# Kernel optimization log

Hardware: AMD Instinct MI355X
Metric: run time of the kernel (lower is better)

Reference implementation:

```python
import jax, jax.numpy as jnp
import numpy as np
import math

D_MODEL = 1024
NUM_HEADS = 16
D_K = D_MODEL // NUM_HEADS
B, NQ, NK = 2, 2048, 2048


def setup_inputs() -> dict:
    key = jax.random.key(0)
    ks = jax.random.split(key, 14)
    s = 1.0 / math.sqrt(D_MODEL)
    inp = {
        "query": jax.random.normal(ks[0], (B, NQ, D_MODEL), jnp.float32),
        "key": jax.random.normal(ks[1], (B, NK, D_MODEL), jnp.float32),
        "value": jax.random.normal(ks[2], (B, NK, D_MODEL), jnp.float32),
        "mask": jax.random.randint(ks[3], (B, NK), 0, 2, jnp.int32),
        "attn_bias": jax.random.normal(ks[4], (B, NQ, NK), jnp.float32),
        "w_q": jax.random.normal(ks[5], (D_MODEL, D_MODEL), jnp.float32) * s,
        "b_q": jnp.zeros((D_MODEL,), jnp.float32),
        "w_k": jax.random.normal(ks[6], (D_MODEL, D_MODEL), jnp.float32) * s,
        "b_k": jnp.zeros((D_MODEL,), jnp.float32),
        "w_v": jax.random.normal(ks[7], (D_MODEL, D_MODEL), jnp.float32) * s,
        "b_v": jnp.zeros((D_MODEL,), jnp.float32),
        "w_o": jax.random.normal(ks[8], (D_MODEL, D_MODEL), jnp.float32) * s,
        "b_o": jnp.zeros((D_MODEL,), jnp.float32),
    }
    return inp


def reference(query, key, value, mask, attn_bias, w_q, b_q, w_k, b_k, w_v, b_v, w_o, b_o):
    # Linear projections (torch Linear: x @ W^T + b), reshape to [B, H, N, d_k]
    def proj(x, w, b, n):
        return (x @ w.T + b).reshape(x.shape[0], n, NUM_HEADS, D_K).transpose(0, 2, 1, 3)

    Q = proj(query, w_q, b_q, query.shape[1])   # [B,H,Nq,dk]
    K = proj(key, w_k, b_k, key.shape[1])       # [B,H,Nk,dk]
    V = proj(value, w_v, b_v, value.shape[1])   # [B,H,Nk,dk]

    scores = jnp.einsum("bhqd,bhkd->bhqk", Q, K) / math.sqrt(D_K)
    scores = scores + attn_bias[:, None, :, :]           # bias broadcast over heads
    pad = (mask[:, None, None, :] == 0)                   # [B,1,1,Nk]
    scores = jnp.where(pad, jnp.float32(-1e9), scores)
    attn = jax.nn.softmax(scores, axis=-1)                # dropout is identity (eval)
    out = jnp.einsum("bhqk,bhkd->bhqd", attn, V)          # [B,H,Nq,dk]
    out = out.transpose(0, 2, 1, 3).reshape(query.shape[0], query.shape[1], D_MODEL)
    return out @ w_o.T + b_o
```

## Files before the change

kernel.cpp:

```cpp
#include <hip/hip_runtime.h>


typedef short bf16x8 __attribute__((ext_vector_type(8)));
typedef short bf16x4 __attribute__((ext_vector_type(4)));
typedef float f32x4 __attribute__((ext_vector_type(4)));
typedef float f32x16 __attribute__((ext_vector_type(16)));
typedef int i32x4 __attribute__((ext_vector_type(4)));
typedef unsigned short u16;
typedef unsigned short u16x8 __attribute__((ext_vector_type(8)));
typedef unsigned short u16x4 __attribute__((ext_vector_type(4)));

#define MFMA16(a, b, c) __builtin_amdgcn_mfma_f32_16x16x32_bf16((a), (b), (c), 0, 0, 0)
#define MFMA32(a, b, c) __builtin_amdgcn_mfma_f32_32x32x16_bf16((a), (b), (c), 0, 0, 0)
#define GLD16(gp, lp)                                                     \
  __builtin_amdgcn_global_load_lds(                                       \
      (const __attribute__((address_space(1))) void*)(gp),                \
      (__attribute__((address_space(3))) void*)(lp), 16, 0, 0)

#define WAITVM_BAR(N) asm volatile("s_waitcnt vmcnt(" #N ")\ns_barrier" ::: "memory")
#define BAR() asm volatile("s_barrier" ::: "memory")

#if __has_builtin(__builtin_amdgcn_exp2f)
#define EXP2(x) __builtin_amdgcn_exp2f(x)
#else
#define EXP2(x) exp2f(x)
#endif

__device__ __forceinline__ u16 f2bf(float f) {
  union { float f; unsigned u; } v; v.f = f;
  return (u16)((v.u + 0x7fffu + ((v.u >> 16) & 1u)) >> 16);
}
__device__ __forceinline__ unsigned pk2(float x, float y) {
  union { float f; unsigned u; } a, b;
  a.f = x; b.f = y;
  return ((a.u + 0x8000u) >> 16) | ((b.u + 0x8000u) & 0xffff0000u);
}
__device__ __forceinline__ void pl32swap(unsigned& a, unsigned& b) {
  asm("v_permlane32_swap_b32 %0, %1" : "+v"(a), "+v"(b));
}

struct ConvDesc { const float* src; u16* dst; int n; };
struct ConvArgs { ConvDesc d[7]; };

__device__ __forceinline__ void biasprep_body(const float* __restrict__ bias,
                                              const int* __restrict__ mask,
                                              u16* __restrict__ out, int i) {
  const int o0 = i * 16;
  const int rowg = o0 >> 11;
  const int b = rowg >> 11;
  const int off = o0 & 2047;
  const int c = off >> 5;
  const int hi = (off >> 4) & 1;
  const float* src = bias + (size_t)rowg * 2048 + c * 32 + hi * 4;
  const int* msk = mask + b * 2048 + c * 32 + hi * 4;
  u16x8 w0 = {}, w1 = {};
#pragma unroll
  for (int t = 0; t < 4; t++) {
    f32x4 v = *(const f32x4*)(src + t * 8);
    i32x4 m = *(const i32x4*)(msk + t * 8);
#pragma unroll
    for (int j = 0; j < 4; j++) {
      u16 val = (m[j] != 0) ? f2bf(v[j] * 1.44269504f) : (u16)0xFF80;
      if (t < 2) w0[t * 4 + j] = val;
      else       w1[(t - 2) * 4 + j] = val;
    }
  }
  *(u16x8*)(out + o0) = w0;
  *(u16x8*)(out + o0 + 8) = w1;
}

__global__ __launch_bounds__(256)
void k_prep(ConvArgs a, const float* __restrict__ bias,
            const int* __restrict__ mask, u16* __restrict__ bout) {
  if (blockIdx.y == 7) {
    biasprep_body(bias, mask, bout, blockIdx.x * 256 + threadIdx.x);
    return;
  }
  ConvDesc cd = a.d[blockIdx.y];
  int i = (blockIdx.x * 256 + threadIdx.x) * 8;
  if (i >= cd.n) return;
  const float4* s = (const float4*)(cd.src + i);
  float4 f0 = s[0], f1 = s[1];
  u16x8 o;
  o[0] = f2bf(f0.x); o[1] = f2bf(f0.y); o[2] = f2bf(f0.z); o[3] = f2bf(f0.w);
  o[4] = f2bf(f1.x); o[5] = f2bf(f1.y); o[6] = f2bf(f1.z); o[7] = f2bf(f1.w);
  *(u16x8*)(cd.dst + i) = o;
}

__global__ __launch_bounds__(256)
void k_biasprep(const float* __restrict__ bias, const int* __restrict__ mask,
                u16* __restrict__ out) {
  biasprep_body(bias, mask, out, blockIdx.x * 256 + threadIdx.x);
}

template <int MF>
__device__ __forceinline__ void gemm_impl(const u16* __restrict__ A,
                                          const u16* __restrict__ Bw,
                                          const float* __restrict__ bias,
                                          void* __restrict__ outp, int mode,
                                          float oscale) {
  __shared__ u16 As[2][MF * 1024];
  __shared__ u16 Bs[2][4096];
  const int tid = threadIdx.x;
  const int lane = tid & 63;
  const int wv = tid >> 6;
  const int wr = wv >> 1, wc = wv & 1;
  const int m0 = blockIdx.y * (MF * 32), n0 = blockIdx.x * 128;

  f32x4 acc[MF][4] = {};

  const int s0 = tid, s1 = 256 + tid;
  const int r0 = s0 >> 2, c0 = (s0 & 3) ^ (r0 & 3);
  const int r1 = s1 >> 2, c1 = (s1 & 3) ^ (r1 & 3);
  const u16* gA0 = A + (size_t)(m0 + r0) * 1024 + c0 * 8;
  const u16* gA1 = A + (size_t)(m0 + r1) * 1024 + c1 * 8;
  const u16* gB0 = Bw + (size_t)(n0 + r0) * 1024 + c0 * 8;
  const u16* gB1 = Bw + (size_t)(n0 + r1) * 1024 + c1 * 8;
  u16* lA0 = &As[0][(tid & ~63) * 8];
  u16* lB0 = &Bs[0][(tid & ~63) * 8];

  GLD16(gA0, lA0);
  if constexpr (MF == 4) GLD16(gA1, lA0 + 2048);
  GLD16(gB0, lB0);
  GLD16(gB1, lB0 + 2048);
  WAITVM_BAR(0);

#define GSTEP(BUF, K0)                                                     \
  {                                                                        \
    const int nk = ((K0) + 32) & 1023;                                     \
    GLD16(gA0 + nk, lA0 + ((BUF) ^ 1) * (MF * 1024));                      \
    if constexpr (MF == 4)                                                 \
      GLD16(gA1 + nk, lA0 + 2048 + ((BUF) ^ 1) * (MF * 1024));             \
    GLD16(gB0 + nk, lB0 + ((BUF) ^ 1) * 4096);                             \
    GLD16(gB1 + nk, lB0 + 2048 + ((BUF) ^ 1) * 4096);                      \
    if constexpr (MF == 4) { WAITVM_BAR(4); } else { WAITVM_BAR(3); }      \
    bf16x8 af[MF], bfr[4];                                                 \
    _Pragma("unroll")                                                      \
    for (int mi = 0; mi < MF; mi++) {                                      \
      int row = wr * (MF * 16) + mi * 16 + (lane & 15);                    \
      int byt = row * 64 + (((lane >> 4) * 16) ^ ((row & 3) << 4));        \
      af[mi] = *(const bf16x8*)((const char*)&As[BUF][0] + byt);           \
    }                                                                      \
    _Pragma("unroll")                                                      \
    for (int ni = 0; ni < 4; ni++) {                                       \
      int row = wc * 64 + ni * 16 + (lane & 15);                           \
      int byt = row * 64 + (((lane >> 4) * 16) ^ ((row & 3) << 4));        \
      bfr[ni] = *(const bf16x8*)((const char*)&Bs[BUF][0] + byt);          \
    }                                                                      \
    __builtin_amdgcn_s_setprio(1);                                         \
    _Pragma("unroll")                                                      \
    for (int mi = 0; mi < MF; mi++)                                        \
      _Pragma("unroll")                                                    \
      for (int ni = 0; ni < 4; ni++)                                       \
        acc[mi][ni] = MFMA16(af[mi], bfr[ni], acc[mi][ni]);                \
    __builtin_amdgcn_s_setprio(0);                                         \
    BAR();                                                                 \
  }

  for (int k0 = 0; k0 < 1024; k0 += 64) {
    GSTEP(0, k0)
    GSTEP(1, k0 + 32)
  }
#undef GSTEP

#pragma unroll
  for (int ni = 0; ni < 4; ni++) {
    int n = n0 + wc * 64 + ni * 16 + (lane & 15);
    float bv = bias[n];
#pragma unroll
    for (int mi = 0; mi < MF; mi++) {
      int mb = m0 + wr * (MF * 16) + mi * 16 + (lane >> 4) * 4;
      if (mode == 2) {
        float* O = (float*)outp;
#pragma unroll
        for (int r = 0; r < 4; r++)
          O[(size_t)(mb + r) * 1024 + n] = (acc[mi][ni][r] + bv) * oscale;
      } else if (mode == 0) {
        u16* O = (u16*)outp;
        int b = mb >> 11, q = mb & 2047;
        int h = n >> 6, dk = n & 63;
        size_t base = ((size_t)(b * 16 + h) * 2048 + q) * 64 + dk;
#pragma unroll
        for (int r = 0; r < 4; r++)
          O[base + (size_t)r * 64] = f2bf((acc[mi][ni][r] + bv) * oscale);
      } else {
        u16* O = (u16*)outp;
        int b = mb >> 11, kv = mb & 2047;
        int h = n >> 6, dk = n & 63;
        u16x4 pk;
#pragma unroll
        for (int r = 0; r < 4; r++) pk[r] = f2bf((acc[mi][ni][r] + bv) * oscale);
        *(u16x4*)((u16*)O + ((size_t)((b * 16 + h) * 64 + dk)) * 2048 + kv) = pk;
      }
    }
  }
}

struct GemmDesc { const u16* A; const u16* W; const float* bias; void* out;
                  int mode; float oscale; };
struct Gemm3 { GemmDesc d[3]; };

__global__ __launch_bounds__(256, 3) void k_gemm_qkv(Gemm3 g3) {
  GemmDesc gd = g3.d[blockIdx.z];
  gemm_impl<4>(gd.A, gd.W, gd.bias, gd.out, gd.mode, gd.oscale);
}
__global__ __launch_bounds__(256, 2)
void k_gemm_o(const u16* __restrict__ A, const u16* __restrict__ W,
              const float* __restrict__ bias, float* __restrict__ out) {
  gemm_impl<2>(A, W, bias, out, 2, 1.0f);
}

__global__ __launch_bounds__(256, 2)
void k_attn(const u16* __restrict__ Qb, const u16* __restrict__ Kb,
            const u16* __restrict__ Vt, const u16* __restrict__ BiasE,
            u16* __restrict__ Ob) {
  __shared__ u16 Ks[2][128 * 64];
  __shared__ u16 Vs[2][64 * 128];

  const int tid = threadIdx.x, lane = tid & 63, w = tid >> 6;
  const int l31 = lane & 31, hi2 = lane >> 5;
  const int bid = blockIdx.x;
  const int xcd = bid & 7, rr = bid >> 3;
  const int qt = rr & 15;
  const int pr = xcd + 8 * (rr >> 4);
  const int b = pr >> 4, h = pr & 15;
  const int q0 = qt * 128;
  const size_t bh = (size_t)(b * 16 + h);

  const u16* Qrow = Qb + (bh * 2048 + q0 + w * 32 + l31) * 64 + hi2 * 8;
  bf16x8 bq[4];
#pragma unroll
  for (int dc = 0; dc < 4; dc++) bq[dc] = *(const bf16x8*)(Qrow + dc * 16);

  f32x16 acc[2] = {};
  float mrun = -1e30f, lrun = 0.f;

  union PF { unsigned u[4]; bf16x8 v; };
  PF pfe[4], pfo[4];

  const u16* Kg = Kb + bh * 2048 * 64;
  const u16* Vg = Vt + bh * 64 * 2048;
  int rK[4], cK[4], rV[4], cV[4], ldd[4];
#pragma unroll
  for (int i = 0; i < 4; i++) {
    int s = i * 256 + tid;
    rK[i] = s >> 3; cK[i] = (s & 7) ^ (rK[i] & 7);
    rV[i] = s >> 4; cV[i] = (s & 15) ^ (rV[i] & 7);
    ldd[i] = (i * 256 + (tid & ~63)) * 8;
  }
  const int kx = (lane & 7) << 4;

  const u16* brow =
      BiasE + ((size_t)b * 2048 + q0 + w * 32 + l31) * 2048 + hi2 * 16;

#pragma unroll
  for (int i = 0; i < 4; i++)
    GLD16(Kg + (size_t)rK[i] * 64 + cK[i] * 8, &Ks[0][ldd[i]]);
#pragma unroll
  for (int i = 0; i < 4; i++)
    GLD16(Vg + (size_t)rV[i] * 2048 + cV[i] * 8, &Vs[0][ldd[i]]);
  u16x8 bb[4][2];
#pragma unroll
  for (int c = 0; c < 4; c++) {
    bb[c][0] = *(const u16x8*)(brow + c * 32);
    bb[c][1] = *(const u16x8*)(brow + c * 32 + 8);
  }

#define ATTN_STEP(BUF, T, HASPV)                                               \
  {                                                                            \
    WAITVM_BAR(0);      \
    const char* kb = (const char*)&Ks[BUF][0];                                 \
    const char* vprev = (const char*)&Vs[(BUF) ^ 1][0];                        \
    f32x16 sc[4];                                                              \
    __builtin_amdgcn_s_setprio(1);                                             \
    _Pragma("unroll")                                                          \
    for (int c = 0; c < 4; c++) {                                              \
      f32x16 z;                                                                \
      _Pragma("unroll")                                                        \
      for (int r = 0; r < 8; r++)                                              \
        z[r] = __uint_as_float((unsigned)bb[c][0][r] << 16);                   \
      _Pragma("unroll")                                                        \
      for (int r = 0; r < 8; r++)                                              \
        z[8 + r] = __uint_as_float((unsigned)bb[c][1][r] << 16);               \
      const int rowb = (c * 32 + l31) * 128;                                   \
      _Pragma("unroll")                                                        \
      for (int dc = 0; dc < 4; dc++) {                                         \
        bf16x8 ak =                                                            \
            *(const bf16x8*)(kb + rowb + ((dc * 32 + hi2 * 16) ^ kx));         \
        z = MFMA32(ak, bq[dc], z);                                             \
      }                                                                        \
      sc[c] = z;                                                               \
    }                                                                          \
    if (HASPV) {                                                               \
      _Pragma("unroll")                                                        \
      for (int c = 0; c < 4; c++) {                                            \
        _Pragma("unroll")                                                      \
        for (int ds = 0; ds < 2; ds++) {                                       \
          const int vrow = (ds * 32 + l31) * 256;                              \
          bf16x8 ve =                                                          \
              *(const bf16x8*)(vprev + vrow + (((c * 4 + hi2) * 16) ^ kx));    \
          acc[ds] = MFMA32(ve, pfe[c].v, acc[ds]);                             \
          bf16x8 vo =                                                          \
              *(const bf16x8*)(vprev + vrow + (((c * 4 + 2 + hi2) * 16) ^ kx)); \
          acc[ds] = MFMA32(vo, pfo[c].v, acc[ds]);                             \
        }                                                                      \
      }                                                                        \
    }                                                                          \
    __builtin_amdgcn_s_setprio(0);                                             \
    BAR();      \
    if ((T) + 1 < 16) {  \
      const int nkv = ((T) + 1) * 128;                                         \
      _Pragma("unroll")                                                        \
      for (int i = 0; i < 4; i++)                                              \
        GLD16(Kg + (size_t)(nkv + rK[i]) * 64 + cK[i] * 8,                     \
              &Ks[(BUF) ^ 1][ldd[i]]);                                         \
      _Pragma("unroll")                                                        \
      for (int i = 0; i < 4; i++)                                              \
        GLD16(Vg + (size_t)rV[i] * 2048 + nkv + cV[i] * 8,                     \
              &Vs[(BUF) ^ 1][ldd[i]]);                                         \
      _Pragma("unroll")                                                        \
      for (int c = 0; c < 4; c++) {                                            \
        bb[c][0] = *(const u16x8*)(brow + nkv + c * 32);                       \
        bb[c][1] = *(const u16x8*)(brow + nkv + c * 32 + 8);                   \
      }                                                                        \
    }                                                                          \
    float cm[4];                                                               \
    _Pragma("unroll")                                                          \
    for (int c = 0; c < 4; c++) {                                              \
      float t8[8];                                                             \
      _Pragma("unroll")                                                        \
      for (int r = 0; r < 8; r++) t8[r] = fmaxf(sc[c][r], sc[c][r + 8]);       \
      float t4[4];                                                             \
      _Pragma("unroll")                                                        \
      for (int r = 0; r < 4; r++) t4[r] = fmaxf(t8[r], t8[r + 4]);             \
      cm[c] = fmaxf(fmaxf(t4[0], t4[1]), fmaxf(t4[2], t4[3]));                 \
    }                                                                          \
    float tmax = fmaxf(fmaxf(cm[0], cm[1]), fmaxf(cm[2], cm[3]));              \
    tmax = fmaxf(tmax, __shfl_xor(tmax, 32, 64));                              \
    if (__any(tmax > mrun)) {                                                  \
      float mnew = fmaxf(mrun, tmax);                                          \
      float alpha = EXP2(mrun - mnew);                                         \
      mrun = mnew;                                                             \
      lrun *= alpha;                                                           \
      _Pragma("unroll")                                                        \
      for (int ds = 0; ds < 2; ds++)                                           \
        _Pragma("unroll")                                                      \
        for (int r = 0; r < 16; r++) acc[ds][r] *= alpha;                      \
    }                                                                          \
    _Pragma("unroll")                                                          \
    for (int c = 0; c < 4; c++)                                                \
      _Pragma("unroll")                                                        \
      for (int r = 0; r < 16; r++) sc[c][r] = EXP2(sc[c][r] - mrun);           \
    float cs[4];                                                               \
    _Pragma("unroll")                                                          \
    for (int c = 0; c < 4; c++) {                                              \
      float s8[8];                                                             \
      _Pragma("unroll")                                                        \
      for (int r = 0; r < 8; r++) s8[r] = sc[c][r] + sc[c][r + 8];             \
      float s4[4];                                                             \
      _Pragma("unroll")                                                        \
      for (int r = 0; r < 4; r++) s4[r] = s8[r] + s8[r + 4];                   \
      cs[c] = (s4[0] + s4[1]) + (s4[2] + s4[3]);                               \
    }                                                                          \
    float rsum = (cs[0] + cs[1]) + (cs[2] + cs[3]);                            \
    rsum += __shfl_xor(rsum, 32, 64);                                          \
    lrun += rsum;                                                              \
    _Pragma("unroll")                                                          \
    for (int c = 0; c < 4; c++) {                                              \
      unsigned a0 = pk2(sc[c][0], sc[c][1]), b0 = pk2(sc[c][4], sc[c][5]);     \
      unsigned a1 = pk2(sc[c][2], sc[c][3]), b1 = pk2(sc[c][6], sc[c][7]);     \
      unsigned e0 = pk2(sc[c][8], sc[c][9]), f0 = pk2(sc[c][12], sc[c][13]);   \
      unsigned e1 = pk2(sc[c][10], sc[c][11]), f1 = pk2(sc[c][14], sc[c][15]); \
      pl32swap(a0, b0); pl32swap(a1, b1);                                      \
      pl32swap(e0, f0); pl32swap(e1, f1);                                      \
      pfe[c].u[0] = a0; pfe[c].u[1] = a1; pfe[c].u[2] = b0; pfe[c].u[3] = b1;  \
      pfo[c].u[0] = e0; pfo[c].u[1] = e1; pfo[c].u[2] = f0; pfo[c].u[3] = f1;  \
    }                                                                          \
  }

  ATTN_STEP(0, 0, 0)
  ATTN_STEP(1, 1, 1)
  for (int t = 2; t < 16; t += 2) {
    ATTN_STEP(0, t, 1)
    ATTN_STEP(1, t + 1, 1)
  }
#undef ATTN_STEP

  {
    const char* vprev = (const char*)&Vs[1][0];
#pragma unroll
    for (int c = 0; c < 4; c++) {
#pragma unroll
      for (int ds = 0; ds < 2; ds++) {
        const int vrow = (ds * 32 + l31) * 256;
        bf16x8 ve =
            *(const bf16x8*)(vprev + vrow + (((c * 4 + hi2) * 16) ^ kx));
        acc[ds] = MFMA32(ve, pfe[c].v, acc[ds]);
        bf16x8 vo =
            *(const bf16x8*)(vprev + vrow + (((c * 4 + 2 + hi2) * 16) ^ kx));
        acc[ds] = MFMA32(vo, pfo[c].v, acc[ds]);
      }
    }
  }

  float linv = 1.0f / lrun;
  const size_t obase =
      ((size_t)b * 2048 + q0 + w * 32 + l31) * 1024 + h * 64 + hi2 * 4;
#pragma unroll
  for (int ds = 0; ds < 2; ds++)
#pragma unroll
    for (int t = 0; t < 4; t++) {
      u16x4 pk;
#pragma unroll
      for (int j = 0; j < 4; j++) pk[j] = f2bf(acc[ds][t * 4 + j] * linv);
      *(u16x4*)(Ob + obase + ds * 32 + t * 8) = pk;
    }
}

extern "C" void kernel_launch(void* const* d_in, const int* in_sizes, int n_in,
                              void* d_out, int out_size, void* d_ws,
                              size_t ws_size, hipStream_t stream) {
  (void)in_sizes; (void)n_in; (void)out_size;
  const float* q_in = (const float*)d_in[0];
  const float* k_in = (const float*)d_in[1];
  const float* v_in = (const float*)d_in[2];
  const int* mask = (const int*)d_in[3];
  const float* attn_bias = (const float*)d_in[4];
  const float* w_q = (const float*)d_in[5];
  const float* b_q = (const float*)d_in[6];
  const float* w_k = (const float*)d_in[7];
  const float* b_k = (const float*)d_in[8];
  const float* w_v = (const float*)d_in[9];
  const float* b_v = (const float*)d_in[10];
  const float* w_o = (const float*)d_in[11];
  const float* b_o = (const float*)d_in[12];

  const size_t MB = 1u << 20;
  char* ws = (char*)d_ws;
  u16* XQ = (u16*)(ws + 0 * MB);
  u16* XK = (u16*)(ws + 8 * MB);
  u16* XV = (u16*)(ws + 16 * MB);
  u16* WQ = (u16*)(ws + 24 * MB);
  u16* WK = (u16*)(ws + 26 * MB);
  u16* WV = (u16*)(ws + 28 * MB);
  u16* WO = (u16*)(ws + 30 * MB);
  u16* Qb = (u16*)(ws + 32 * MB);
  u16* Kb = (u16*)(ws + 40 * MB);
  u16* Vt = (u16*)(ws + 48 * MB);
  u16* Ob = (u16*)(ws + 56 * MB);
  const bool merged = ws_size >= (size_t)80 * MB;
  u16* BiasE = (u16*)(ws + (merged ? 64 : 0) * MB);

  ConvArgs ca;
  ca.d[0] = {q_in, XQ, 4096 * 1024};
  ca.d[1] = {k_in, XK, 4096 * 1024};
  ca.d[2] = {v_in, XV, 4096 * 1024};
  ca.d[3] = {w_q, WQ, 1024 * 1024};
  ca.d[4] = {w_k, WK, 1024 * 1024};
  ca.d[5] = {w_v, WV, 1024 * 1024};
  ca.d[6] = {w_o, WO, 1024 * 1024};
  k_prep<<<dim3(2048, merged ? 8 : 7), 256, 0, stream>>>(ca, attn_bias, mask,
                                                         BiasE);

  const float QSCALE = 0.125f * 1.44269504f;
  Gemm3 g3;
  g3.d[0] = {XQ, WQ, b_q, (void*)Qb, 0, QSCALE};
  g3.d[1] = {XK, WK, b_k, (void*)Kb, 0, 1.0f};
  g3.d[2] = {XV, WV, b_v, (void*)Vt, 1, 1.0f};
  k_gemm_qkv<<<dim3(8, 32, 3), 256, 0, stream>>>(g3);

  if (!merged) k_biasprep<<<2048, 256, 0, stream>>>(attn_bias, mask, BiasE);

  k_attn<<<512, 256, 0, stream>>>(Qb, Kb, Vt, BiasE, Ob);

  k_gemm_o<<<dim3(8, 64), 256, 0, stream>>>(Ob, WO, b_o, (float*)d_out);
}
```

Measured before the change: 152.2 us.

## Triple-buffer V tiles and drop mid-step barrier in attention pipeline

Gives V a third LDS buffer and rotates K/V buffers so each step's next-tile K/V loads are issued before the softmax work without a second barrier. The wait before each step drops from vmcnt(0) to vmcnt(4). The online-softmax rescale now fires only when the running max grows by more than 8, which skips most rescales at some risk to exp2 range. This trades extra LDS, which may lower occupancy, for fewer stalls, and correctness now hinges on the buffer rotation and vmcnt accounting.

```diff
diff --git a/kernel.cpp b/kernel.cpp
--- a/kernel.cpp
+++ b/kernel.cpp
@@ -215,7 +215,7 @@
             const u16* __restrict__ Vt, const u16* __restrict__ BiasE,
             u16* __restrict__ Ob) {
   __shared__ u16 Ks[2][128 * 64];
-  __shared__ u16 Vs[2][64 * 128];
+  __shared__ u16 Vs[3][64 * 128];
 
   const int tid = threadIdx.x, lane = tid & 63, w = tid >> 6;
   const int l31 = lane & 31, hi2 = lane >> 5;
@@ -253,24 +253,24 @@
   const u16* brow =
       BiasE + ((size_t)b * 2048 + q0 + w * 32 + l31) * 2048 + hi2 * 16;
 
-#pragma unroll
-  for (int i = 0; i < 4; i++)
-    GLD16(Kg + (size_t)rK[i] * 64 + cK[i] * 8, &Ks[0][ldd[i]]);
-#pragma unroll
-  for (int i = 0; i < 4; i++)
-    GLD16(Vg + (size_t)rV[i] * 2048 + cV[i] * 8, &Vs[0][ldd[i]]);
   u16x8 bb[4][2];
 #pragma unroll
   for (int c = 0; c < 4; c++) {
     bb[c][0] = *(const u16x8*)(brow + c * 32);
     bb[c][1] = *(const u16x8*)(brow + c * 32 + 8);
   }
-
-#define ATTN_STEP(BUF, T, HASPV)                                               \
+#pragma unroll
+  for (int i = 0; i < 4; i++)
+    GLD16(Kg + (size_t)rK[i] * 64 + cK[i] * 8, &Ks[0][ldd[i]]);
+#pragma unroll
+  for (int i = 0; i < 4; i++)
+    GLD16(Vg + (size_t)rV[i] * 2048 + cV[i] * 8, &Vs[0][ldd[i]]);
+
+#define ATTN_STEP(KB, VP, VN, T, HASPV, STAGE)                                 \
   {                                                                            \
-    WAITVM_BAR(0);      \
-    const char* kb = (const char*)&Ks[BUF][0];                                 \
-    const char* vprev = (const char*)&Vs[(BUF) ^ 1][0];                        \
+    WAITVM_BAR(4);           \
+    const char* kb = (const char*)&Ks[KB][0];                                  \
+    const char* vprev = (const char*)&Vs[VP][0];                               \
     f32x16 sc[4];                                                              \
     __builtin_amdgcn_s_setprio(1);                                             \
     _Pragma("unroll")                                                          \
@@ -291,7 +291,7 @@
       }                                                                        \
       sc[c] = z;                                                               \
     }                                                                          \
-    if (HASPV) {                                                               \
+    if (HASPV) {         \
       _Pragma("unroll")                                                        \
       for (int c = 0; c < 4; c++) {                                            \
         _Pragma("unroll")                                                      \
@@ -307,22 +307,21 @@
       }                                                                        \
     }                                                                          \
     __builtin_amdgcn_s_setprio(0);                                             \
-    BAR();      \
-    if ((T) + 1 < 16) {  \
+    if (STAGE) {     \
       const int nkv = ((T) + 1) * 128;                                         \
-      _Pragma("unroll")                                                        \
-      for (int i = 0; i < 4; i++)                                              \
-        GLD16(Kg + (size_t)(nkv + rK[i]) * 64 + cK[i] * 8,                     \
-              &Ks[(BUF) ^ 1][ldd[i]]);                                         \
-      _Pragma("unroll")                                                        \
-      for (int i = 0; i < 4; i++)                                              \
-        GLD16(Vg + (size_t)rV[i] * 2048 + nkv + cV[i] * 8,                     \
-              &Vs[(BUF) ^ 1][ldd[i]]);                                         \
       _Pragma("unroll")                                                        \
       for (int c = 0; c < 4; c++) {                                            \
         bb[c][0] = *(const u16x8*)(brow + nkv + c * 32);                       \
         bb[c][1] = *(const u16x8*)(brow + nkv + c * 32 + 8);                   \
       }                                                                        \
+      _Pragma("unroll")                                                        \
+      for (int i = 0; i < 4; i++)                                              \
+        GLD16(Kg + (size_t)(nkv + rK[i]) * 64 + cK[i] * 8,                     \
+              &Ks[(KB) ^ 1][ldd[i]]);                                          \
+      _Pragma("unroll")                                                        \
+      for (int i = 0; i < 4; i++)                                              \
+        GLD16(Vg + (size_t)rV[i] * 2048 + nkv + cV[i] * 8,                     \
+              &Vs[VN][ldd[i]]);                                                \
     }                                                                          \
     float cm[4];                                                               \
     _Pragma("unroll")                                                          \
@@ -337,7 +336,7 @@
     }                                                                          \
     float tmax = fmaxf(fmaxf(cm[0], cm[1]), fmaxf(cm[2], cm[3]));              \
     tmax = fmaxf(tmax, __shfl_xor(tmax, 32, 64));                              \
-    if (__any(tmax > mrun)) {                                                  \
+    if (__any(tmax > mrun + 8.f)) {           \
       float mnew = fmaxf(mrun, tmax);                                          \
       float alpha = EXP2(mrun - mnew);                                         \
       mrun = mnew;                                                             \
@@ -378,16 +377,27 @@
     }                                                                          \
   }
 
-  ATTN_STEP(0, 0, 0)
-  ATTN_STEP(1, 1, 1)
-  for (int t = 2; t < 16; t += 2) {
-    ATTN_STEP(0, t, 1)
-    ATTN_STEP(1, t + 1, 1)
-  }
+  ATTN_STEP(0, 0, 1, 0, 0, 1)
+  ATTN_STEP(1, 0, 2, 1, 1, 1)
+  ATTN_STEP(0, 1, 0, 2, 1, 1)
+  ATTN_STEP(1, 2, 1, 3, 1, 1)
+  ATTN_STEP(0, 0, 2, 4, 1, 1)
+  ATTN_STEP(1, 1, 0, 5, 1, 1)
+  ATTN_STEP(0, 2, 1, 6, 1, 1)
+  ATTN_STEP(1, 0, 2, 7, 1, 1)
+  ATTN_STEP(0, 1, 0, 8, 1, 1)
+  ATTN_STEP(1, 2, 1, 9, 1, 1)
+  ATTN_STEP(0, 0, 2, 10, 1, 1)
+  ATTN_STEP(1, 1, 0, 11, 1, 1)
+  ATTN_STEP(0, 2, 1, 12, 1, 1)
+  ATTN_STEP(1, 0, 2, 13, 1, 1)
+  ATTN_STEP(0, 1, 0, 14, 1, 1)
+  ATTN_STEP(1, 2, 0, 15, 1, 0)
 #undef ATTN_STEP
 
+  WAITVM_BAR(0);
   {
-    const char* vprev = (const char*)&Vs[1][0];
+    const char* vprev = (const char*)&Vs[0][0];
 #pragma unroll
     for (int c = 0; c < 4; c++) {
 #pragma unroll
```

New measurement: 150.2 us. Within noise of the previous version (-1.3%).
